# Performance work log

Measured on AMD Instinct MI355X. Metric: run time of the kernel, lower is better.

The kernel has to match this reference:

```python
import jax, jax.numpy as jnp
import numpy as np

NVEC = [100000, 100000, 100000]
OFFSETS = np.concatenate([[0], np.cumsum(NVEC)[:-1]]).astype(np.int32)  # [0,100000,200000]
DIM = 64
B = 500000
HID = 50
IN_DIM = len(NVEC) * DIM + 1  # 193


def setup_inputs() -> dict:
    key = jax.random.key(0)
    ks = jax.random.split(key, 7)
    batch_ind = jax.random.randint(ks[0], (B, len(NVEC)), 0, NVEC[0], dtype=jnp.int32)
    batch_t = jax.random.uniform(ks[1], (B,), dtype=jnp.float32)
    U = jax.random.uniform(ks[2], (int(np.sum(NVEC)), DIM), dtype=jnp.float32)
    W1 = jax.random.normal(ks[3], (IN_DIM, HID), dtype=jnp.float32) * 0.1
    b1 = jax.random.normal(ks[4], (HID,), dtype=jnp.float32) * 0.1
    W2 = jax.random.normal(ks[5], (HID, 1), dtype=jnp.float32) * 0.1
    b2 = jax.random.normal(ks[6], (1,), dtype=jnp.float32) * 0.1
    return {"batch_ind": batch_ind, "batch_t": batch_t, "U": U,
            "W1": W1, "b1": b1, "W2": W2, "b2": b2}


def reference(batch_ind, batch_t, U, W1, b1, W2, b2):
    # per-mode gather: offset each mode's index into the concatenated U table
    offs = jnp.asarray(OFFSETS)  # [nmod]
    idx = batch_ind + offs[None, :]          # [B, nmod] global row ids
    emb = U[idx]                              # [B, nmod, D] single fused gather
    X = jnp.concatenate([emb.reshape(emb.shape[0], -1),
                         batch_t[:, None]], axis=1)  # [B, nmod*D+1]
    h = jnp.tanh(X @ W1 + b1)                 # [B, 50]
    return h @ W2 + b2                        # [B, 1]
```

## Files before the change

kernel.cpp:

```cpp
#include <hip/hip_runtime.h>
#include <hip/hip_bf16.h>

using bf16x8 = __attribute__((ext_vector_type(8))) short;
using f16x8  = __attribute__((ext_vector_type(8))) _Float16;
using f16x4  = __attribute__((ext_vector_type(4))) _Float16;
using f32x4  = __attribute__((ext_vector_type(4))) float;

#define THREADS   256
#define NROWS_U   300000
#define WS_NEED   (NROWS_U * 64 * 2)
#define NTILES_PC 18750
#define NB_PC     768
#define NB_MAIN   2048
#define NITERS_M  15625

__device__ __forceinline__ short f2bf(float f) {
    __hip_bfloat16 h = __float2bfloat16(f);
    return __builtin_bit_cast(short, h);
}

__device__ __forceinline__ bf16x8 cvt8(float4 a, float4 b) {
    bf16x8 r;
    r[0] = f2bf(a.x); r[1] = f2bf(a.y); r[2] = f2bf(a.z); r[3] = f2bf(a.w);
    r[4] = f2bf(b.x); r[5] = f2bf(b.y); r[6] = f2bf(b.z); r[7] = f2bf(b.w);
    return r;
}

__global__ __launch_bounds__(THREADS) void pc_kernel(
    const float* __restrict__ U,
    const float* __restrict__ W1,
    _Float16*    __restrict__ V)
{
    __shared__ short bsh[24][64][8];
    for (int e = threadIdx.x; e < 24 * 64; e += THREADS) {
        int f = e >> 6, l = e & 63;
        int m = f >> 3, rem = f & 7, nt = rem >> 1, ks = rem & 1;
        int n  = nt * 16 + (l & 15);
        int k0 = m * 64 + ks * 32 + ((l >> 4) << 3);
        bf16x8 v;
#pragma unroll
        for (int j = 0; j < 8; ++j) {
            float w = (n < 50) ? W1[(k0 + j) * 50 + n] : 0.f;
            v[j] = f2bf(w);
        }
        *(bf16x8*)(&bsh[f][l][0]) = v;
    }
    __syncthreads();

    const int lane = threadIdx.x & 63;
    const int g    = lane >> 4;
    const int ncol = lane & 15;
    const int nwv  = NB_PC * (THREADS / 64);
    const int wid  = blockIdx.x * (THREADS / 64) + (threadIdx.x >> 6);

    int tile = wid;
    if (tile >= NTILES_PC) return;

    float4 r0, r1, r2, r3;
    {
        const float* p = U + (size_t)(tile * 16 + ncol) * 64 + g * 8;
        r0 = ((const float4*)p)[0];        r1 = ((const float4*)p)[1];
        r2 = ((const float4*)(p + 32))[0]; r3 = ((const float4*)(p + 32))[1];
    }

    for (; tile < NTILES_PC; tile += nwv) {
        const int nxt = tile + nwv;

        float4 s0, s1, s2, s3;
        if (nxt < NTILES_PC) {
            const float* p = U + (size_t)(nxt * 16 + ncol) * 64 + g * 8;
            s0 = ((const float4*)p)[0];        s1 = ((const float4*)p)[1];
            s2 = ((const float4*)(p + 32))[0]; s3 = ((const float4*)(p + 32))[1];
        }

        const int mode = tile / 6250;
        const int base = tile * 16;
        bf16x8 A0 = cvt8(r0, r1);
        bf16x8 A1 = cvt8(r2, r3);

        f32x4 acc[4];
#pragma unroll
        for (int nt = 0; nt < 4; ++nt) acc[nt] = (f32x4){0.f, 0.f, 0.f, 0.f};
#pragma unroll
        for (int nt = 0; nt < 4; ++nt) {
            bf16x8 B0 = *(const bf16x8*)(&bsh[mode * 8 + nt * 2 + 0][lane][0]);
            bf16x8 B1 = *(const bf16x8*)(&bsh[mode * 8 + nt * 2 + 1][lane][0]);
            acc[nt] = __builtin_amdgcn_mfma_f32_16x16x32_bf16(A0, B0, acc[nt], 0, 0, 0);
            acc[nt] = __builtin_amdgcn_mfma_f32_16x16x32_bf16(A1, B1, acc[nt], 0, 0, 0);
        }

#pragma unroll
        for (int r = 0; r < 4; ++r) {
            f16x4 pk;
#pragma unroll
            for (int nt = 0; nt < 4; ++nt) pk[nt] = (_Float16)acc[nt][r];
            *(f16x4*)(V + (size_t)(base + g * 4 + r) * 64 + ncol * 4) = pk;
        }

        r0 = s0; r1 = s1; r2 = s2; r3 = s3;
    }
}

__global__ __launch_bounds__(THREADS) void etl_main(
    const int*      __restrict__ bi,
    const float*    __restrict__ t,
    const _Float16* __restrict__ V,
    const float*    __restrict__ W1,
    const float*    __restrict__ b1,
    const float*    __restrict__ W2,
    const float*    __restrict__ b2,
    float*          __restrict__ out)
{
    const int lane = threadIdx.x & 63;
    const int r8   = lane >> 3;
    const int c    = lane & 7;

    float w192r[8], b1r[8], w2r[8];
#pragma unroll
    for (int j = 0; j < 8; ++j) {
        int pos = c * 8 + j;
        int n = (pos & 3) * 16 + (pos >> 2);
        bool vld = n < 50;
        w192r[j] = vld ? W1[192 * 50 + n] : 0.f;
        b1r[j]   = vld ? b1[n] : 0.f;
        w2r[j]   = vld ? W2[n] : 0.f;
    }
    const float b2v = b2[0];

    const int nwaves = NB_MAIN * (THREADS / 64);
    for (int it = blockIdx.x * (THREADS / 64) + (threadIdx.x >> 6);
         it < NITERS_M; it += nwaves) {
        const int base = it * 32;

        int id[4][3];
#pragma unroll
        for (int u = 0; u < 4; ++u) {
            int r = base + u * 8 + r8;
#pragma unroll
            for (int m = 0; m < 3; ++m)
                id[u][m] = bi[r * 3 + m] + m * 100000;
        }

        f16x8 va[4][3];
#pragma unroll
        for (int u = 0; u < 4; ++u)
#pragma unroll
            for (int m = 0; m < 3; ++m)
                va[u][m] = *(const f16x8*)(V + (size_t)id[u][m] * 64 + c * 8);

        float tv[4];
#pragma unroll
        for (int u = 0; u < 4; ++u) tv[u] = t[base + u * 8 + r8];

#pragma unroll
        for (int u = 0; u < 4; ++u) {
            float acc = 0.f;
#pragma unroll
            for (int j = 0; j < 8; ++j) {
                float h = (float)va[u][0][j] + (float)va[u][1][j] +
                          (float)va[u][2][j] + tv[u] * w192r[j] + b1r[j];
                float e = __expf(2.f * h);
                acc += (1.f - 2.f * __builtin_amdgcn_rcpf(e + 1.f)) * w2r[j];
            }
            acc += __shfl_xor(acc, 1, 64);
            acc += __shfl_xor(acc, 2, 64);
            acc += __shfl_xor(acc, 4, 64);
            if (c == 0) out[base + u * 8 + r8] = acc + b2v;
        }
    }
}

__global__ __launch_bounds__(THREADS) void etl_f32(
    const int*   __restrict__ bi,
    const float* __restrict__ t,
    const float* __restrict__ U,
    const float* __restrict__ W1,
    const float* __restrict__ b1,
    const float* __restrict__ W2,
    const float* __restrict__ b2,
    float*       __restrict__ out)
{
    __shared__ short bsh[24][64][8];
    for (int e = threadIdx.x; e < 24 * 64; e += THREADS) {
        int f = e >> 6, l = e & 63;
        int nt = f / 6, ks = f - nt * 6;
        int n  = nt * 16 + (l & 15);
        int k0 = ks * 32 + ((l >> 4) << 3);
        bf16x8 v;
#pragma unroll
        for (int j = 0; j < 8; ++j) {
            float w = (n < 50) ? W1[(k0 + j) * 50 + n] : 0.f;
            v[j] = f2bf(w);
        }
        *(bf16x8*)(&bsh[f][l][0]) = v;
    }
    __syncthreads();

    const int lane = threadIdx.x & 63;
    const int g    = lane >> 4;
    const int ncol = lane & 15;

    bf16x8 Bf[24];
#pragma unroll
    for (int f = 0; f < 24; ++f) Bf[f] = *(const bf16x8*)(&bsh[f][lane][0]);

    float w192[4], b1r[4], w2r[4];
#pragma unroll
    for (int nt = 0; nt < 4; ++nt) {
        int n = nt * 16 + ncol;
        bool vld = (n < 50);
        w192[nt] = vld ? W1[192 * 50 + n] : 0.f;
        b1r[nt]  = vld ? b1[n] : 0.f;
        w2r[nt]  = vld ? W2[n] : 0.f;
    }
    const float b2v = b2[0];

    const int nwaves = 768 * (THREADS / 64);
    const int wid    = blockIdx.x * (THREADS / 64) + (threadIdx.x >> 6);

    for (int tile = wid; tile < 31250; tile += nwaves) {
        const int base = tile * 16;
        const int row  = base + ncol;
        int i0 = bi[row * 3 + 0];
        int i1 = bi[row * 3 + 1] + 100000;
        int i2 = bi[row * 3 + 2] + 200000;

        bf16x8 A[6];
        const float* p0 = U + (size_t)i0 * 64 + g * 8;
        const float* p1 = U + (size_t)i1 * 64 + g * 8;
        const float* p2 = U + (size_t)i2 * 64 + g * 8;
        A[0] = cvt8(((const float4*)p0)[0], ((const float4*)p0)[1]);
        A[1] = cvt8(((const float4*)(p0 + 32))[0], ((const float4*)(p0 + 32))[1]);
        A[2] = cvt8(((const float4*)p1)[0], ((const float4*)p1)[1]);
        A[3] = cvt8(((const float4*)(p1 + 32))[0], ((const float4*)(p1 + 32))[1]);
        A[4] = cvt8(((const float4*)p2)[0], ((const float4*)p2)[1]);
        A[5] = cvt8(((const float4*)(p2 + 32))[0], ((const float4*)(p2 + 32))[1]);

        f32x4 acc[4];
#pragma unroll
        for (int nt = 0; nt < 4; ++nt) acc[nt] = (f32x4){0.f, 0.f, 0.f, 0.f};
#pragma unroll
        for (int ks = 0; ks < 6; ++ks) {
#pragma unroll
            for (int nt = 0; nt < 4; ++nt) {
                acc[nt] = __builtin_amdgcn_mfma_f32_16x16x32_bf16(
                    A[ks], Bf[nt * 6 + ks], acc[nt], 0, 0, 0);
            }
        }

        float4 tv = *(const float4*)(t + base + g * 4);
        float tarr[4] = {tv.x, tv.y, tv.z, tv.w};
        float part[4] = {0.f, 0.f, 0.f, 0.f};
#pragma unroll
        for (int nt = 0; nt < 4; ++nt) {
#pragma unroll
            for (int r = 0; r < 4; ++r) {
                float pre = acc[nt][r] + tarr[r] * w192[nt] + b1r[nt];
                float e  = __expf(2.f * pre);
                float h  = 1.f - 2.f * __builtin_amdgcn_rcpf(e + 1.f);
                part[r] += h * w2r[nt];
            }
        }
#pragma unroll
        for (int r = 0; r < 4; ++r) {
#pragma unroll
            for (int m = 1; m < 16; m <<= 1)
                part[r] += __shfl_xor(part[r], m, 64);
        }
        if (ncol == 0) {
            float4 o = make_float4(part[0] + b2v, part[1] + b2v,
                                   part[2] + b2v, part[3] + b2v);
            *(float4*)(out + base + g * 4) = o;
        }
    }
}

extern "C" void kernel_launch(void* const* d_in, const int* in_sizes, int n_in,
                              void* d_out, int out_size, void* d_ws, size_t ws_size,
                              hipStream_t stream) {
    const int*   bi = (const int*)  d_in[0];
    const float* t  = (const float*)d_in[1];
    const float* U  = (const float*)d_in[2];
    const float* W1 = (const float*)d_in[3];
    const float* b1 = (const float*)d_in[4];
    const float* W2 = (const float*)d_in[5];
    const float* b2 = (const float*)d_in[6];
    float* out = (float*)d_out;

    if (ws_size >= (size_t)WS_NEED) {
        _Float16* V = (_Float16*)d_ws;
        pc_kernel<<<NB_PC, THREADS, 0, stream>>>(U, W1, V);
        etl_main<<<NB_MAIN, THREADS, 0, stream>>>(bi, t, V, W1, b1, W2, b2, out);
    } else {
        etl_f32<<<768, THREADS, 0, stream>>>(bi, t, U, W1, b1, W2, b2, out);
    }
}
```

Before: 61.63 us.

## Hold W1 fragments in registers and give each wave a contiguous tile chunk

The precompute kernel no longer stages all of W1 into shared memory, which needed a block-wide load and sync before any work. Each wave now loads only the W1 fragment for its current mode straight into registers and reloads it only when the mode changes. Work is split into contiguous chunks of four tiles per wave, with more blocks and a launch-bounds occupancy hint, instead of a grid-stride loop. This removes LDS setup and LDS reads per tile, at the cost of redundant per-wave W1 global loads, more register pressure, and less prefetch overlap per wave.

```diff
diff --git a/kernel.cpp b/kernel.cpp
--- a/kernel.cpp
+++ b/kernel.cpp
@@ -10,7 +10,8 @@
 #define NROWS_U   300000
 #define WS_NEED   (NROWS_U * 64 * 2)
 #define NTILES_PC 18750
-#define NB_PC     768
+#define CPW       4
+#define NB_PC     1172
 #define NB_MAIN   2048
 #define NITERS_M  15625
 
@@ -26,69 +27,88 @@
     return r;
 }
 
-__global__ __launch_bounds__(THREADS) void pc_kernel(
+__global__ __launch_bounds__(THREADS, 4) void pc_kernel(
     const float* __restrict__ U,
     const float* __restrict__ W1,
     _Float16*    __restrict__ V)
 {
-    __shared__ short bsh[24][64][8];
-    for (int e = threadIdx.x; e < 24 * 64; e += THREADS) {
-        int f = e >> 6, l = e & 63;
-        int m = f >> 3, rem = f & 7, nt = rem >> 1, ks = rem & 1;
-        int n  = nt * 16 + (l & 15);
-        int k0 = m * 64 + ks * 32 + ((l >> 4) << 3);
-        bf16x8 v;
-#pragma unroll
-        for (int j = 0; j < 8; ++j) {
-            float w = (n < 50) ? W1[(k0 + j) * 50 + n] : 0.f;
-            v[j] = f2bf(w);
-        }
-        *(bf16x8*)(&bsh[f][l][0]) = v;
-    }
-    __syncthreads();
-
     const int lane = threadIdx.x & 63;
     const int g    = lane >> 4;
     const int ncol = lane & 15;
-    const int nwv  = NB_PC * (THREADS / 64);
     const int wid  = blockIdx.x * (THREADS / 64) + (threadIdx.x >> 6);
 
-    int tile = wid;
-    if (tile >= NTILES_PC) return;
+    const int t0 = wid * CPW;
+    if (t0 >= NTILES_PC) return;
+    const int tend = (t0 + CPW < NTILES_PC) ? t0 + CPW : NTILES_PC;
+
+    bf16x8 Bf[8];
+    int cur_mode = t0 / 6250;
+    {
+        const int m = cur_mode;
+#pragma unroll
+        for (int nt = 0; nt < 4; ++nt) {
+            const int n = nt * 16 + ncol;
+            const bool vld = n < 50;
+#pragma unroll
+            for (int ks = 0; ks < 2; ++ks) {
+                bf16x8 v;
+#pragma unroll
+                for (int j = 0; j < 8; ++j) {
+                    float w = vld ? W1[(m * 64 + ks * 32 + g * 8 + j) * 50 + n] : 0.f;
+                    v[j] = f2bf(w);
+                }
+                Bf[nt * 2 + ks] = v;
+            }
+        }
+    }
 
     float4 r0, r1, r2, r3;
     {
-        const float* p = U + (size_t)(tile * 16 + ncol) * 64 + g * 8;
+        const float* p = U + (size_t)(t0 * 16 + ncol) * 64 + g * 8;
         r0 = ((const float4*)p)[0];        r1 = ((const float4*)p)[1];
         r2 = ((const float4*)(p + 32))[0]; r3 = ((const float4*)(p + 32))[1];
     }
 
-    for (; tile < NTILES_PC; tile += nwv) {
-        const int nxt = tile + nwv;
-
+    for (int tile = t0; tile < tend; ++tile) {
         float4 s0, s1, s2, s3;
-        if (nxt < NTILES_PC) {
-            const float* p = U + (size_t)(nxt * 16 + ncol) * 64 + g * 8;
+        if (tile + 1 < tend) {
+            const float* p = U + (size_t)((tile + 1) * 16 + ncol) * 64 + g * 8;
             s0 = ((const float4*)p)[0];        s1 = ((const float4*)p)[1];
             s2 = ((const float4*)(p + 32))[0]; s3 = ((const float4*)(p + 32))[1];
         }
 
         const int mode = tile / 6250;
-        const int base = tile * 16;
+        if (mode != cur_mode) {
+            cur_mode = mode;
+#pragma unroll
+            for (int nt = 0; nt < 4; ++nt) {
+                const int n = nt * 16 + ncol;
+                const bool vld = n < 50;
+#pragma unroll
+                for (int ks = 0; ks < 2; ++ks) {
+                    bf16x8 v;
+#pragma unroll
+                    for (int j = 0; j < 8; ++j) {
+                        float w = vld ? W1[(mode * 64 + ks * 32 + g * 8 + j) * 50 + n] : 0.f;
+                        v[j] = f2bf(w);
+                    }
+                    Bf[nt * 2 + ks] = v;
+                }
+            }
+        }
+
         bf16x8 A0 = cvt8(r0, r1);
         bf16x8 A1 = cvt8(r2, r3);
-
         f32x4 acc[4];
 #pragma unroll
         for (int nt = 0; nt < 4; ++nt) acc[nt] = (f32x4){0.f, 0.f, 0.f, 0.f};
 #pragma unroll
         for (int nt = 0; nt < 4; ++nt) {
-            bf16x8 B0 = *(const bf16x8*)(&bsh[mode * 8 + nt * 2 + 0][lane][0]);
-            bf16x8 B1 = *(const bf16x8*)(&bsh[mode * 8 + nt * 2 + 1][lane][0]);
-            acc[nt] = __builtin_amdgcn_mfma_f32_16x16x32_bf16(A0, B0, acc[nt], 0, 0, 0);
-            acc[nt] = __builtin_amdgcn_mfma_f32_16x16x32_bf16(A1, B1, acc[nt], 0, 0, 0);
-        }
-
+            acc[nt] = __builtin_amdgcn_mfma_f32_16x16x32_bf16(A0, Bf[nt * 2 + 0], acc[nt], 0, 0, 0);
+            acc[nt] = __builtin_amdgcn_mfma_f32_16x16x32_bf16(A1, Bf[nt * 2 + 1], acc[nt], 0, 0, 0);
+        }
+
+        const int base = tile * 16;
 #pragma unroll
         for (int r = 0; r < 4; ++r) {
             f16x4 pk;
```

New measurement: 58.04 us. 1.06x faster.
